# Performance work log

Hardware: AMD Instinct MI355X
Metric: run time of the kernel (lower is better)

Reference implementation:

```python
import jax, jax.numpy as jnp
import numpy as np

EMB = 1024
HEADS = 16
HEAD_DIM = EMB // HEADS


def setup_inputs() -> dict:
    key = jax.random.key(0)
    ks = jax.random.split(key, 9)
    s = 1.0 / np.sqrt(EMB)
    return {
        "x": jax.random.normal(ks[0], (2, 2048, EMB), dtype=jnp.float32),
        "wq": jax.random.uniform(ks[1], (EMB, EMB), jnp.float32, -s, s),
        "bq": jax.random.uniform(ks[2], (EMB,), jnp.float32, -s, s),
        "wk": jax.random.uniform(ks[3], (EMB, EMB), jnp.float32, -s, s),
        "bk": jax.random.uniform(ks[4], (EMB,), jnp.float32, -s, s),
        "wv": jax.random.uniform(ks[5], (EMB, EMB), jnp.float32, -s, s),
        "bv": jax.random.uniform(ks[6], (EMB,), jnp.float32, -s, s),
        "wo": jax.random.uniform(ks[7], (EMB, EMB), jnp.float32, -s, s),
        "bo": jax.random.uniform(ks[8], (EMB,), jnp.float32, -s, s),
    }


def reference(x, wq, bq, wk, bk, wv, bv, wo, bo):
    b, n, d = x.shape
    h, hd = HEADS, HEAD_DIM
    # projections (weights stored as (in, out) = torch W.T)
    q = (x @ wq + bq).reshape(b, n, h, hd).transpose(0, 2, 1, 3)  # b h n hd
    k = (x @ wk + bk).reshape(b, n, h, hd).transpose(0, 2, 1, 3)
    v = (x @ wv + bv).reshape(b, n, h, hd).transpose(0, 2, 1, 3)
    scale = 1.0 / np.sqrt(hd).astype(np.float32)
    attn = jnp.einsum("bhqd,bhkd->bhqk", q, k) * scale
    attn = jax.nn.softmax(attn, axis=-1)
    out = jnp.einsum("bhqk,bhkd->bhqd", attn, v)
    out = out.transpose(0, 2, 1, 3).reshape(b, n, d)
    return out @ wo + bo
```

## Files before the change

kernel.cpp:

```cpp
#include <hip/hip_runtime.h>
#include <stdint.h>

typedef __attribute__((ext_vector_type(8))) short v8s;
typedef __attribute__((ext_vector_type(4))) short v4s;
typedef __attribute__((ext_vector_type(4))) float v4f;
typedef __attribute__((ext_vector_type(2))) unsigned v2u;
typedef unsigned short u16;

#define EMB 1024
#define TOKS 4096
#define NSEQ 2048
#define NH 16
#define HD 64

__device__ __forceinline__ u16 f2bf(float f) {
    unsigned u = __builtin_bit_cast(unsigned, f);
    u += 0x7fffu + ((u >> 16) & 1u);
    return (u16)(u >> 16);
}
__device__ __forceinline__ float bf2f(u16 h) {
    unsigned u = ((unsigned)h) << 16;
    return __builtin_bit_cast(float, u);
}
__device__ __forceinline__ float exp2_fast(float x) {
#if __has_builtin(__builtin_amdgcn_exp2f)
    return __builtin_amdgcn_exp2f(x);
#else
    return exp2f(x);
#endif
}
__device__ __forceinline__ unsigned pack_hi16(unsigned t0, unsigned t1) {
#if __has_builtin(__builtin_amdgcn_perm)
    return __builtin_amdgcn_perm(t1, t0, 0x07060302u);
#else
    return (t0 >> 16) | (t1 & 0xffff0000u);
#endif
}

__device__ __forceinline__ void gll16(const void* g, void* l) {
    __builtin_amdgcn_global_load_lds(
        (const __attribute__((address_space(1))) unsigned int*)g,
        (__attribute__((address_space(3))) unsigned int*)l, 16, 0, 0);
}

__global__ void k_convx(const float* __restrict__ x, u16* __restrict__ xhi) {
    int i = (blockIdx.x * 256 + threadIdx.x) * 4;
    v4f v = *(const v4f*)(x + i);
    v4s h;
#pragma unroll
    for (int j = 0; j < 4; j++) h[j] = (short)f2bf(v[j]);
    *(v4s*)(xhi + i) = h;
}

__global__ void k_convw(const float* __restrict__ w0, const float* __restrict__ w1,
                        const float* __restrict__ w2, const float* __restrict__ w3,
                        u16* __restrict__ whi) {
    __shared__ float t[64][65];
    int z = blockIdx.z;
    const float* w = (z == 0) ? w0 : (z == 1) ? w1 : (z == 2) ? w2 : w3;
    int r0 = blockIdx.x * 64, c0 = blockIdx.y * 64;
    int tr = threadIdx.x >> 4, tc = (threadIdx.x & 15) * 4;
#pragma unroll
    for (int i = 0; i < 4; i++) {
        int row = tr + i * 16;
        v4f v = *(const v4f*)(w + (size_t)(r0 + row) * EMB + c0 + tc);
#pragma unroll
        for (int j = 0; j < 4; j++) t[row][tc + j] = v[j];
    }
    __syncthreads();
    u16* dz = whi + (size_t)z * EMB * EMB;
#pragma unroll
    for (int i = 0; i < 4; i++) {
        int orow = tr + i * 16;
        v4s h;
#pragma unroll
        for (int j = 0; j < 4; j++) h[j] = (short)f2bf(t[tc + j][orow]);
        *(v4s*)(dz + (size_t)(c0 + orow) * EMB + r0 + tc) = h;
    }
}

__global__ __launch_bounds__(256, 2) void k_gemm(
    const u16* __restrict__ A, const u16* __restrict__ B0,
    const float* __restrict__ b0, const float* __restrict__ b1, const float* __restrict__ b2,
    u16* __restrict__ outBF, u16* __restrict__ vT) {
    __shared__ u16 sA[8192], sB[8192];
    int z = blockIdx.z;
    const u16* B = B0 + (size_t)z * EMB * EMB;
    const float* bias = (z == 0) ? b0 : (z == 1) ? b1 : b2;
    int f = blockIdx.y * 32 + blockIdx.x;
    int fp = (f & 7) * 32 + (f >> 3);
    int m0 = (fp & 31) * 128, n0 = (fp >> 5) * 128;
    int tid = threadIdx.x, lane = tid & 63, w = tid >> 6;
    int wm = w >> 1, wn = w & 1;
    int lr = lane & 15, lk = lane >> 4;
    int srow8 = lane >> 3, kc8 = lane & 7;
    v4f z4 = {0.f, 0.f, 0.f, 0.f};
    v4f acc[4][4];
#pragma unroll
    for (int mi = 0; mi < 4; mi++)
#pragma unroll
        for (int ni = 0; ni < 4; ni++) acc[mi][ni] = z4;

    int c0 = (lk ^ (lr & 7)) * 8, c1 = ((4 + lk) ^ (lr & 7)) * 8;
    for (int kt = 0; kt < 16; ++kt) {
#pragma unroll
        for (int ii = 0; ii < 4; ii++) {
            int it = w * 4 + ii;
            int row = it * 8 + srow8;
            int kc = kc8 ^ (row & 7);
            gll16(&A[(size_t)(m0 + row) * EMB + kt * 64 + kc * 8], &sA[it * 512]);
            gll16(&B[(size_t)(n0 + row) * EMB + kt * 64 + kc * 8], &sB[it * 512]);
        }
        __syncthreads();
        v8s af[4][2], bf[4][2];
#pragma unroll
        for (int i = 0; i < 4; i++) {
            int ra = (wm * 64 + i * 16 + lr) * 64;
            af[i][0] = *(const v8s*)(&sA[ra + c0]);
            af[i][1] = *(const v8s*)(&sA[ra + c1]);
            int rb = (wn * 64 + i * 16 + lr) * 64;
            bf[i][0] = *(const v8s*)(&sB[rb + c0]);
            bf[i][1] = *(const v8s*)(&sB[rb + c1]);
        }
#pragma unroll
        for (int mi = 0; mi < 4; mi++)
#pragma unroll
            for (int ni = 0; ni < 4; ni++) {
                acc[mi][ni] = __builtin_amdgcn_mfma_f32_16x16x32_bf16(af[mi][0], bf[ni][0], acc[mi][ni], 0, 0, 0);
                acc[mi][ni] = __builtin_amdgcn_mfma_f32_16x16x32_bf16(af[mi][1], bf[ni][1], acc[mi][ni], 0, 0, 0);
            }
        __syncthreads();
    }

#pragma unroll
    for (int mi = 0; mi < 4; mi++) {
#pragma unroll
        for (int ni = 0; ni < 4; ni++) {
            int col = n0 + wn * 64 + ni * 16 + lr;
            float bv = bias[col];
            if (z == 2) {
                int h = col >> 6, d = col & 63;
                v4s pk;
#pragma unroll
                for (int r = 0; r < 4; r++) pk[r] = (short)f2bf(acc[mi][ni][r] + bv);
                int row = m0 + wm * 64 + mi * 16 + lk * 4;
                int bb = row >> 11, nn = row & 2047;
                *(v4s*)(&vT[((size_t)(bb * NH + h) * HD + d) * NSEQ + nn]) = pk;
            } else {
#pragma unroll
                for (int r = 0; r < 4; r++) {
                    int row = m0 + wm * 64 + mi * 16 + lk * 4 + r;
                    float val = acc[mi][ni][r] + bv;
                    if (z == 0) val *= 0.18033688011112042f;
                    int bb = row >> 11, nn = row & 2047, h = col >> 6, d = col & 63;
                    size_t idx = (((size_t)(bb * NH + h)) * NSEQ + nn) * HD + d;
                    (outBF + (size_t)z * TOKS * EMB)[idx] = f2bf(val);
                }
            }
        }
    }
}

__global__ __launch_bounds__(256, 2) void k_gemmO(
    const u16* __restrict__ A, const u16* __restrict__ B,
    const float* __restrict__ bias, float* __restrict__ outF) {
    __shared__ u16 sA[4096], sB[8192];
    int f = blockIdx.y * 64 + blockIdx.x;
    int fp = (f & 7) * 64 + (f >> 3);
    int m0 = (fp & 63) * 64, n0 = (fp >> 6) * 128;
    int tid = threadIdx.x, lane = tid & 63, w = tid >> 6;
    int wm = w >> 1, wn = w & 1;
    int lr = lane & 15, lk = lane >> 4;
    int srow8 = lane >> 3, kc8 = lane & 7;
    v4f z4 = {0.f, 0.f, 0.f, 0.f};
    v4f acc[2][4];
#pragma unroll
    for (int mi = 0; mi < 2; mi++)
#pragma unroll
        for (int ni = 0; ni < 4; ni++) acc[mi][ni] = z4;

    int c0 = (lk ^ (lr & 7)) * 8, c1 = ((4 + lk) ^ (lr & 7)) * 8;
    for (int kt = 0; kt < 16; ++kt) {
#pragma unroll
        for (int ii = 0; ii < 2; ii++) {
            int it = w * 2 + ii;
            int row = it * 8 + srow8;
            int kc = kc8 ^ (row & 7);
            gll16(&A[(size_t)(m0 + row) * EMB + kt * 64 + kc * 8], &sA[it * 512]);
        }
#pragma unroll
        for (int ii = 0; ii < 4; ii++) {
            int it = w * 4 + ii;
            int row = it * 8 + srow8;
            int kc = kc8 ^ (row & 7);
            gll16(&B[(size_t)(n0 + row) * EMB + kt * 64 + kc * 8], &sB[it * 512]);
        }
        __syncthreads();
        v8s af[2][2], bf[4][2];
#pragma unroll
        for (int i = 0; i < 2; i++) {
            int ra = (wm * 32 + i * 16 + lr) * 64;
            af[i][0] = *(const v8s*)(&sA[ra + c0]);
            af[i][1] = *(const v8s*)(&sA[ra + c1]);
        }
#pragma unroll
        for (int i = 0; i < 4; i++) {
            int rb = (wn * 64 + i * 16 + lr) * 64;
            bf[i][0] = *(const v8s*)(&sB[rb + c0]);
            bf[i][1] = *(const v8s*)(&sB[rb + c1]);
        }
#pragma unroll
        for (int mi = 0; mi < 2; mi++)
#pragma unroll
            for (int ni = 0; ni < 4; ni++) {
                acc[mi][ni] = __builtin_amdgcn_mfma_f32_16x16x32_bf16(af[mi][0], bf[ni][0], acc[mi][ni], 0, 0, 0);
                acc[mi][ni] = __builtin_amdgcn_mfma_f32_16x16x32_bf16(af[mi][1], bf[ni][1], acc[mi][ni], 0, 0, 0);
            }
        __syncthreads();
    }
#pragma unroll
    for (int mi = 0; mi < 2; mi++)
#pragma unroll
        for (int ni = 0; ni < 4; ni++) {
            int col = n0 + wn * 64 + ni * 16 + lr;
            float bv = bias[col];
#pragma unroll
            for (int r = 0; r < 4; r++) {
                int row = m0 + wm * 32 + mi * 16 + lk * 4 + r;
                outF[(size_t)row * EMB + col] = acc[mi][ni][r] + bv;
            }
        }
}

__global__ __launch_bounds__(256, 4) void k_attn(
    const u16* __restrict__ Q, const u16* __restrict__ K, const u16* __restrict__ Vt,
    u16* __restrict__ O) {
    __shared__ u16 sK[2][4096];
    __shared__ u16 sP[4096];
    float* sL = (float*)&sK[0][0];
    int tid = threadIdx.x, lane = tid & 63, w = tid >> 6;
    int lr = lane & 15, lk = lane >> 4;
    int bid = blockIdx.x;
    int qi = (bid >> 3) & 31;
    int bh = (bid & 7) | (((bid >> 8) & 3) << 3);
    int q0 = qi * 64;

    const u16* Qb = Q + ((size_t)bh * NSEQ + q0) * HD;
    v8s qf[4][2];
#pragma unroll
    for (int qg = 0; qg < 4; qg++)
#pragma unroll
        for (int c = 0; c < 2; c++)
            qf[qg][c] = *(const v8s*)(Qb + (qg * 16 + lr) * HD + c * 32 + lk * 8);

    const u16* Kb = K + (size_t)bh * NSEQ * HD;
    const u16* Vb = Vt + ((size_t)bh * HD + w * 16 + lr) * NSEQ;
    v4f z4 = {0.f, 0.f, 0.f, 0.f};
    v4f oacc[4] = {z4, z4, z4, z4};
    float l_part[4] = {0.f, 0.f, 0.f, 0.f};
    int srow8 = lane >> 3, kc8 = lane & 7;

#pragma unroll
    for (int ii = 0; ii < 2; ii++) {
        int it = w * 2 + ii;
        int row = it * 8 + srow8;
        int kc = kc8 ^ (row & 7);
        gll16(&Kb[(size_t)row * HD + kc * 8], &sK[0][it * 512]);
    }
    __syncthreads();

    int kread0 = (w * 16 + lr) * 64 + ((lk ^ (lr & 7)) * 8);
    int kread1 = (w * 16 + lr) * 64 + (((4 + lk) ^ (lr & 7)) * 8);
    int pwbase = (((w * 2 + (lk >> 1)) ^ (lr & 7)) << 2) + (lk & 1) * 2;

    for (int t = 0; t < 32; ++t) {
        int cur = t & 1;
        if (t < 31) {
#pragma unroll
            for (int ii = 0; ii < 2; ii++) {
                int it = w * 2 + ii;
                int row = it * 8 + srow8;
                int kc = kc8 ^ (row & 7);
                gll16(&Kb[(size_t)((t + 1) * 64 + row) * HD + kc * 8], &sK[cur ^ 1][it * 512]);
            }
        }
        v8s vb0 = *(const v8s*)(Vb + t * 64 + lk * 8);
        v8s vb1 = *(const v8s*)(Vb + t * 64 + 32 + lk * 8);

        v8s kf0 = *(const v8s*)(&sK[cur][kread0]);
        v8s kf1 = *(const v8s*)(&sK[cur][kread1]);
        v4f sacc[4];
#pragma unroll
        for (int qg = 0; qg < 4; qg++) {
            v4f a = z4;
            a = __builtin_amdgcn_mfma_f32_16x16x32_bf16(kf0, qf[qg][0], a, 0, 0, 0);
            a = __builtin_amdgcn_mfma_f32_16x16x32_bf16(kf1, qf[qg][1], a, 0, 0, 0);
            sacc[qg] = a;
        }
        float pv[4][4];
#pragma unroll
        for (int qg = 0; qg < 4; qg++) {
            pv[qg][0] = exp2_fast(sacc[qg][0]);
            pv[qg][1] = exp2_fast(sacc[qg][1]);
            pv[qg][2] = exp2_fast(sacc[qg][2]);
            pv[qg][3] = exp2_fast(sacc[qg][3]);
            l_part[qg] += (pv[qg][0] + pv[qg][1]) + (pv[qg][2] + pv[qg][3]);
        }
        __syncthreads();
#pragma unroll
        for (int qg = 0; qg < 4; qg++) {
            unsigned pk0 = pack_hi16(__builtin_bit_cast(unsigned, pv[qg][0]),
                                     __builtin_bit_cast(unsigned, pv[qg][1]));
            unsigned pk1 = pack_hi16(__builtin_bit_cast(unsigned, pv[qg][2]),
                                     __builtin_bit_cast(unsigned, pv[qg][3]));
            int q = qg * 16 + lr;
            v2u pk = {pk0, pk1};
            *(v2u*)(&sP[(q * 32 + pwbase) * 2]) = pk;
        }
        __syncthreads();
#pragma unroll
        for (int qg = 0; qg < 4; qg++) {
            int q = qg * 16 + lr;
            v8s pf0 = *(const v8s*)(&sP[(q * 32 + ((lk ^ (lr & 7)) << 2)) * 2]);
            v8s pf1 = *(const v8s*)(&sP[(q * 32 + (((4 + lk) ^ (lr & 7)) << 2)) * 2]);
            oacc[qg] = __builtin_amdgcn_mfma_f32_16x16x32_bf16(pf0, vb0, oacc[qg], 0, 0, 0);
            oacc[qg] = __builtin_amdgcn_mfma_f32_16x16x32_bf16(pf1, vb1, oacc[qg], 0, 0, 0);
        }
    }
#pragma unroll
    for (int qg = 0; qg < 4; qg++) {
        l_part[qg] += __shfl_xor(l_part[qg], 16);
        l_part[qg] += __shfl_xor(l_part[qg], 32);
    }
    __syncthreads();
    if (lk == 0) {
#pragma unroll
        for (int qg = 0; qg < 4; qg++) sL[(qg * 16 + lr) * 4 + w] = l_part[qg];
    }
    __syncthreads();
    int bb = bh >> 4, h = bh & 15;
    int dcol = h * 64 + w * 16 + lr;
#pragma unroll
    for (int qg = 0; qg < 4; qg++) {
#pragma unroll
        for (int r = 0; r < 4; r++) {
            int qq = qg * 16 + lk * 4 + r;
            v4f lv = *(const v4f*)(&sL[qq * 4]);
            float inv = 1.f / ((lv[0] + lv[1]) + (lv[2] + lv[3]));
            O[(size_t)(bb * NSEQ + q0 + qq) * EMB + dcol] = f2bf(oacc[qg][r] * inv);
        }
    }
}

extern "C" void kernel_launch(void* const* d_in, const int* in_sizes, int n_in,
                              void* d_out, int out_size, void* d_ws, size_t ws_size,
                              hipStream_t stream) {
    const float* x  = (const float*)d_in[0];
    const float* wq = (const float*)d_in[1];
    const float* bq = (const float*)d_in[2];
    const float* wk = (const float*)d_in[3];
    const float* bk = (const float*)d_in[4];
    const float* wv = (const float*)d_in[5];
    const float* bv = (const float*)d_in[6];
    const float* wo = (const float*)d_in[7];
    const float* bo = (const float*)d_in[8];

    char* W = (char*)d_ws;
    u16* xhi = (u16*)(W);
    u16* whi = (u16*)(W + 8388608);
    u16* qkv = (u16*)(W + 16777216);
    u16* Obf = (u16*)(W + 41943040);

    u16* Qp  = qkv;
    u16* Kp  = qkv + 4194304;
    u16* Vtp = qkv + 8388608;

    k_convx<<<4096, 256, 0, stream>>>(x, xhi);
    k_convw<<<dim3(16, 16, 4), 256, 0, stream>>>(wq, wk, wv, wo, whi);
    k_gemm<<<dim3(32, 8, 3), 256, 0, stream>>>(xhi, whi, bq, bk, bv, qkv, Vtp);
    k_attn<<<dim3(1024), 256, 0, stream>>>(Qp, Kp, Vtp, Obf);
    k_gemmO<<<dim3(64, 8), 256, 0, stream>>>(Obf, whi + (size_t)3 * EMB * EMB,
                                             bo, (float*)d_out);
}
```

Measured before the change: 111.7 us.

## Split attention over two KV halves and combine partials in a new kernel

The attention kernel now splits the key/value sequence into two halves, doubling the block count so each block processes 16 KV tiles instead of 32. Each block writes unnormalized bf16 partial outputs and per-row sum partials to workspace. A new combine kernel adds the two partials and divides by the total softmax denominator. This is meant to raise parallelism and shorten each block's serial loop. In exchange it adds an extra launch, extra global traffic for the partial buffers, and an extra bf16 rounding of the partial outputs.

```diff
diff --git a/kernel.cpp b/kernel.cpp
--- a/kernel.cpp
+++ b/kernel.cpp
@@ -234,16 +234,18 @@
 
 __global__ __launch_bounds__(256, 4) void k_attn(
     const u16* __restrict__ Q, const u16* __restrict__ K, const u16* __restrict__ Vt,
-    u16* __restrict__ O) {
+    u16* __restrict__ Opart, float* __restrict__ Lpart) {
     __shared__ u16 sK[2][4096];
     __shared__ u16 sP[4096];
     float* sL = (float*)&sK[0][0];
     int tid = threadIdx.x, lane = tid & 63, w = tid >> 6;
     int lr = lane & 15, lk = lane >> 4;
     int bid = blockIdx.x;
-    int qi = (bid >> 3) & 31;
-    int bh = (bid & 7) | (((bid >> 8) & 3) << 3);
+    int kvh = (bid >> 3) & 1;
+    int qi = (bid >> 4) & 31;
+    int bh = (bid & 7) | (((bid >> 9) & 3) << 3);
     int q0 = qi * 64;
+    int t0 = kvh * 16;
 
     const u16* Qb = Q + ((size_t)bh * NSEQ + q0) * HD;
     v8s qf[4][2];
@@ -265,7 +267,7 @@
         int it = w * 2 + ii;
         int row = it * 8 + srow8;
         int kc = kc8 ^ (row & 7);
-        gll16(&Kb[(size_t)row * HD + kc * 8], &sK[0][it * 512]);
+        gll16(&Kb[(size_t)(t0 * 64 + row) * HD + kc * 8], &sK[0][it * 512]);
     }
     __syncthreads();
 
@@ -273,9 +275,9 @@
     int kread1 = (w * 16 + lr) * 64 + (((4 + lk) ^ (lr & 7)) * 8);
     int pwbase = (((w * 2 + (lk >> 1)) ^ (lr & 7)) << 2) + (lk & 1) * 2;
 
-    for (int t = 0; t < 32; ++t) {
+    for (int t = t0; t < t0 + 16; ++t) {
         int cur = t & 1;
-        if (t < 31) {
+        if (t < t0 + 15) {
 #pragma unroll
             for (int ii = 0; ii < 2; ii++) {
                 int it = w * 2 + ii;
@@ -340,16 +342,37 @@
     __syncthreads();
     int bb = bh >> 4, h = bh & 15;
     int dcol = h * 64 + w * 16 + lr;
+    u16* Op = Opart + (size_t)kvh * TOKS * EMB;
+    float* Lp = Lpart + (size_t)kvh * 32 * NSEQ + (size_t)bh * NSEQ;
 #pragma unroll
     for (int qg = 0; qg < 4; qg++) {
 #pragma unroll
         for (int r = 0; r < 4; r++) {
             int qq = qg * 16 + lk * 4 + r;
-            v4f lv = *(const v4f*)(&sL[qq * 4]);
-            float inv = 1.f / ((lv[0] + lv[1]) + (lv[2] + lv[3]));
-            O[(size_t)(bb * NSEQ + q0 + qq) * EMB + dcol] = f2bf(oacc[qg][r] * inv);
-        }
-    }
+            Op[(size_t)(bb * NSEQ + q0 + qq) * EMB + dcol] = f2bf(oacc[qg][r]);
+            if (w == 0 && lr == 0) {
+                v4f lv = *(const v4f*)(&sL[qq * 4]);
+                Lp[q0 + qq] = (lv[0] + lv[1]) + (lv[2] + lv[3]);
+            }
+        }
+    }
+}
+
+__global__ void k_comb(const u16* __restrict__ Opart, const float* __restrict__ Lpart,
+                       u16* __restrict__ O) {
+    int i = (blockIdx.x * 256 + threadIdx.x) * 4;
+    int tok = i >> 10, col = i & 1023;
+    int bb = tok >> 11, nn = tok & 2047, h = col >> 6;
+    int bhi = bb * NH + h;
+    float inv = 1.f / (Lpart[(size_t)bhi * NSEQ + nn] +
+                       Lpart[(size_t)32 * NSEQ + (size_t)bhi * NSEQ + nn]);
+    v4s a = *(const v4s*)(Opart + i);
+    v4s b = *(const v4s*)(Opart + (size_t)TOKS * EMB + i);
+    v4s o;
+#pragma unroll
+    for (int j = 0; j < 4; j++)
+        o[j] = (short)f2bf((bf2f((u16)a[j]) + bf2f((u16)b[j])) * inv);
+    *(v4s*)(O + i) = o;
 }
 
 extern "C" void kernel_launch(void* const* d_in, const int* in_sizes, int n_in,
@@ -366,10 +389,12 @@
     const float* bo = (const float*)d_in[8];
 
     char* W = (char*)d_ws;
-    u16* xhi = (u16*)(W);
-    u16* whi = (u16*)(W + 8388608);
-    u16* qkv = (u16*)(W + 16777216);
-    u16* Obf = (u16*)(W + 41943040);
+    u16* xhi   = (u16*)(W);
+    u16* whi   = (u16*)(W + 8388608);
+    u16* qkv   = (u16*)(W + 16777216);
+    u16* Obf   = (u16*)(W + 41943040);
+    u16* Opart = (u16*)(W + 50331648);
+    float* Lpart = (float*)(W + 67108864);
 
     u16* Qp  = qkv;
     u16* Kp  = qkv + 4194304;
@@ -378,7 +403,8 @@
     k_convx<<<4096, 256, 0, stream>>>(x, xhi);
     k_convw<<<dim3(16, 16, 4), 256, 0, stream>>>(wq, wk, wv, wo, whi);
     k_gemm<<<dim3(32, 8, 3), 256, 0, stream>>>(xhi, whi, bq, bk, bv, qkv, Vtp);
-    k_attn<<<dim3(1024), 256, 0, stream>>>(Qp, Kp, Vtp, Obf);
+    k_attn<<<dim3(2048), 256, 0, stream>>>(Qp, Kp, Vtp, Opart, Lpart);
+    k_comb<<<4096, 256, 0, stream>>>(Opart, Lpart, Obf);
     k_gemmO<<<dim3(64, 8), 256, 0, stream>>>(Obf, whi + (size_t)3 * EMB * EMB,
                                              bo, (float*)d_out);
 }
```

Result: slower. 123.1 us (+10.3%).
